# Kernel tuning notes

Hardware: AMD Instinct MI355X
Metric: run time of the kernel (lower is better)

## Reference

```python
import jax, jax.numpy as jnp
import numpy as np

Q, B, S, D, N = 4, 8, 1024, 768, 1024
H = 2 * D // 3  # 512, from encoder hidden = 2*dim//3
TAU = 1e-6      # eval-mode gumbel temperature
BN_EPS = 1e-5


def setup_inputs() -> dict:
    key = jax.random.key(0)
    ks = jax.random.split(key, 12)
    rn = lambda k, sh, sc=0.02: (jax.random.normal(k, sh, jnp.float32) * sc)
    u = jax.random.uniform(ks[0], (Q, B, S, N), jnp.float32, 1e-9, 1.0)
    return {
        "x": jax.random.normal(ks[1], (B, S, D), jnp.float32),
        "codebooks": rn(ks[2], (Q, N, D), 0.05),
        # posterior MLPs (per-quantizer, stacked over Q): Linear+BN(eval)+ReLU x2
        "pW1": rn(ks[3], (Q, D, H)), "pb1": jnp.zeros((Q, H)),
        "pg1": jnp.ones((Q, H)), "pbe1": jnp.zeros((Q, H)),
        "pm1": jnp.zeros((Q, H)), "pv1": jnp.ones((Q, H)),
        "pW2": rn(ks[4], (Q, H, N)), "pb2": jnp.zeros((Q, N)),
        "pg2": jnp.ones((Q, N)), "pbe2": jnp.zeros((Q, N)),
        "pm2": jnp.zeros((Q, N)), "pv2": jnp.ones((Q, N)),
        # shared decoder: D -> 2D -> D
        "dW1": rn(ks[5], (D, 2 * D)), "db1": jnp.zeros((2 * D,)),
        "dg1": jnp.ones((2 * D,)), "dbe1": jnp.zeros((2 * D,)),
        "dm1": jnp.zeros((2 * D,)), "dv1": jnp.ones((2 * D,)),
        "dW2": rn(ks[6], (2 * D, D)), "db2": jnp.zeros((D,)),
        "dg2": jnp.ones((D,)), "dbe2": jnp.zeros((D,)),
        "dm2": jnp.zeros((D,)), "dv2": jnp.ones((D,)),
        # precomputed gumbel noise (deterministic replacement for F.gumbel_softmax sampling)
        "gumbel": -jnp.log(-jnp.log(u)),
    }


def _bn(x, g, b, m, v):
    # eval-mode BatchNorm1d over the last (channel) axis
    return (x - m) * (g * jax.lax.rsqrt(v + BN_EPS)) + b


def _blk(x, W, b, g, be, m, v):
    return jax.nn.relu(_bn(x @ W + b, g, be, m, v))


def reference(x, codebooks, pW1, pb1, pg1, pbe1, pm1, pv1,
              pW2, pb2, pg2, pbe2, pm2, pv2,
              dW1, db1, dg1, dbe1, dm1, dv1,
              dW2, db2, dg2, dbe2, dm2, dv2, gumbel):
    residual = x
    quantized_out = jnp.zeros_like(x)
    indices, latent_losses, entropies, zs = [], [], [], []
    for i in range(Q):
        h = _blk(residual, pW1[i], pb1[i], pg1[i], pbe1[i], pm1[i], pv1[i])
        z = _blk(h, pW2[i], pb2[i], pg2[i], pbe2[i], pm2[i], pv2[i])  # [B,S,N]
        qy = jax.nn.softmax(z, axis=2)
        entropy = -jnp.sum(qy * jnp.log(qy + 1e-10), axis=-1)          # [B,S]
        latent = qy * jnp.log(qy * N + 1e-10)                           # [B,S,N]
        # gumbel-softmax, hard=True (straight-through)
        logits = (z + gumbel[i]) / TAU
        y_soft = jax.nn.softmax(logits, axis=2)
        idx = jnp.argmax(logits, axis=2)                                # [B,S]
        y_hard = jax.nn.one_hot(idx, N, dtype=z.dtype)
        one_hot = y_hard + y_soft - jax.lax.stop_gradient(y_soft)
        z_q = jnp.einsum('bsn,nd->bsd', one_hot, codebooks[i])
        residual = residual - jax.lax.stop_gradient(z_q)
        quantized_out = quantized_out + z_q
        indices.append(idx); latent_losses.append(latent)
        zs.append(z); entropies.append(entropy)
    h = _blk(quantized_out, dW1, db1, dg1, dbe1, dm1, dv1)
    xhat = _blk(h, dW2, db2, dg2, dbe2, dm2, dv2)
    return (xhat,
            jnp.stack(entropies, axis=0),
            jnp.stack(latent_losses, axis=0),
            jnp.stack(indices, axis=0),
            jnp.stack(zs, axis=0))
```

## Files before the change

kernel.cpp:

```cpp
#include <hip/hip_runtime.h>

namespace {

constexpr int QN = 4;
constexpr int MR = 8192;
constexpr int DD = 768;
constexpr int HH = 512;
constexpr int NN = 1024;
constexpr float DELTA = 0.008f;

typedef __attribute__((ext_vector_type(8))) __bf16 bf16x8;
typedef __attribute__((ext_vector_type(4))) __bf16 bf16x4;
typedef __attribute__((ext_vector_type(4))) float  f32x4;

#define GL2LDS(g, l) __builtin_amdgcn_global_load_lds( \
    (const __attribute__((address_space(1))) void*)(g), \
    (__attribute__((address_space(3))) void*)(l), 16, 0, 0)

__global__ __launch_bounds__(256)
void wcvt(const float* __restrict__ src, __bf16* __restrict__ dst, int K, int N)
{
    __shared__ float tile[32][33];
    const size_t bo = (size_t)blockIdx.z * K * N;
    const int n0 = blockIdx.x * 32, k0 = blockIdx.y * 32;
    const int tx = threadIdx.x, ty = threadIdx.y;
    #pragma unroll
    for (int i = 0; i < 4; ++i)
        tile[ty + 8 * i][tx] = src[bo + (size_t)(k0 + ty + 8 * i) * N + n0 + tx];
    __syncthreads();
    #pragma unroll
    for (int i = 0; i < 4; ++i)
        dst[bo + (size_t)(n0 + ty + 8 * i) * K + k0 + tx] = (__bf16)tile[tx][ty + 8 * i];
}

__global__ __launch_bounds__(256)
void acvt(const float* __restrict__ src, __bf16* __restrict__ dst,
          int* __restrict__ cnt)
{
    if (blockIdx.x == 0 && threadIdx.x < QN) cnt[threadIdx.x] = 0;
    const size_t i = ((size_t)blockIdx.x * 256 + threadIdx.x) * 8;
    float4 a = *(const float4*)(src + i);
    float4 b = *(const float4*)(src + i + 4);
    bf16x8 o;
    o[0] = (__bf16)a.x; o[1] = (__bf16)a.y; o[2] = (__bf16)a.z; o[3] = (__bf16)a.w;
    o[4] = (__bf16)b.x; o[5] = (__bf16)b.y; o[6] = (__bf16)b.z; o[7] = (__bf16)b.w;
    *(bf16x8*)(dst + i) = o;
}

template<int OUTBF>
__global__ __launch_bounds__(256)
void gemm_mfma(const __bf16* __restrict__ A, const __bf16* __restrict__ BT,
               const float* __restrict__ bias, const float* __restrict__ gam,
               const float* __restrict__ beta, const float* __restrict__ mean,
               const float* __restrict__ var,
               float* __restrict__ C32, __bf16* __restrict__ Cbf,
               int N_, int K_)
{
    __shared__ __bf16 smem[24576];

    const int t   = threadIdx.x;
    const int bn0 = blockIdx.x * 128;
    const int bm0 = blockIdx.y * 128;
    const int l    = t & 63, w = t >> 6;
    const int lm   = l & 15, quad = l >> 4;
    const int mrow = (w & 1) * 64, ncol = (w >> 1) * 64;

    const int sA0 = t, sA1 = t + 256;
    const int mA0 = sA0 >> 2, qA0 = ((sA0 & 3) - (mA0 >> 1)) & 3;
    const int mA1 = sA1 >> 2, qA1 = ((sA1 & 3) - (mA1 >> 1)) & 3;
    const size_t gA0 = (size_t)(bm0 + mA0) * K_ + qA0 * 8;
    const size_t gA1 = (size_t)(bm0 + mA1) * K_ + qA1 * 8;
    const size_t gB0 = (size_t)(bn0 + mA0) * K_ + qA0 * 8;
    const size_t gB1 = (size_t)(bn0 + mA1) * K_ + qA1 * 8;

    f32x4 acc[4][4] = {};

    int aslot[4], bslot[4];
    #pragma unroll
    for (int i = 0; i < 4; ++i) {
        int m = mrow + i * 16 + lm;
        aslot[i] = m * 4 + ((quad + (m >> 1)) & 3);
        int n = ncol + i * 16 + lm;
        bslot[i] = n * 4 + ((quad + (n >> 1)) & 3);
    }

    const int nk = K_ >> 5;

    {
        __bf16* As = smem;
        __bf16* Bs = smem + 4096;
        GL2LDS(A  + gA0, As + sA0 * 8);
        GL2LDS(A  + gA1, As + sA1 * 8);
        GL2LDS(BT + gB0, Bs + sA0 * 8);
        GL2LDS(BT + gB1, Bs + sA1 * 8);
        As = smem + 8192;
        Bs = As + 4096;
        GL2LDS(A  + gA0 + 32, As + sA0 * 8);
        GL2LDS(A  + gA1 + 32, As + sA1 * 8);
        GL2LDS(BT + gB0 + 32, Bs + sA0 * 8);
        GL2LDS(BT + gB1 + 32, Bs + sA1 * 8);
    }

    int bc = 0;
    for (int ks = 0; ks < nk; ++ks) {
        if (ks + 1 < nk) asm volatile("s_waitcnt vmcnt(4)" ::: "memory");
        else             asm volatile("s_waitcnt vmcnt(0)" ::: "memory");
        __builtin_amdgcn_s_barrier();
        asm volatile("" ::: "memory");

        if (ks + 2 < nk) {
            int sb = bc + 2; if (sb >= 3) sb -= 3;
            __bf16* Asn = smem + sb * 8192;
            __bf16* Bsn = Asn + 4096;
            const size_t ko = (size_t)(ks + 2) * 32;
            GL2LDS(A  + gA0 + ko, Asn + sA0 * 8);
            GL2LDS(A  + gA1 + ko, Asn + sA1 * 8);
            GL2LDS(BT + gB0 + ko, Bsn + sA0 * 8);
            GL2LDS(BT + gB1 + ko, Bsn + sA1 * 8);
        }

        const __bf16* As = smem + bc * 8192;
        const __bf16* Bs = As + 4096;
        bf16x8 af[4], bfv[4];
        #pragma unroll
        for (int i = 0; i < 4; ++i) {
            af[i]  = *(const bf16x8*)(As + aslot[i] * 8);
            bfv[i] = *(const bf16x8*)(Bs + bslot[i] * 8);
        }
        #pragma unroll
        for (int mt = 0; mt < 4; ++mt)
            #pragma unroll
            for (int nt = 0; nt < 4; ++nt)
                acc[mt][nt] = __builtin_amdgcn_mfma_f32_16x16x32_bf16(
                    af[mt], bfv[nt], acc[mt][nt], 0, 0, 0);

        asm volatile("s_waitcnt lgkmcnt(0)" ::: "memory");
        bc = (bc == 2) ? 0 : bc + 1;
    }

    float sc[4], sh[4]; int cn[4];
    #pragma unroll
    for (int nt = 0; nt < 4; ++nt) {
        int c = bn0 + ncol + nt * 16 + lm;
        cn[nt] = c;
        float s = gam[c] * rsqrtf(var[c] + 1e-5f);
        sc[nt] = s;
        sh[nt] = (bias[c] - mean[c]) * s + beta[c];
    }
    #pragma unroll
    for (int mt = 0; mt < 4; ++mt) {
        int r0 = bm0 + mrow + mt * 16 + quad * 4;
        #pragma unroll
        for (int nt = 0; nt < 4; ++nt) {
            #pragma unroll
            for (int reg = 0; reg < 4; ++reg) {
                float v = fmaxf(0.f, fmaf(acc[mt][nt][reg], sc[nt], sh[nt]));
                size_t off = (size_t)(r0 + reg) * N_ + cn[nt];
                if (OUTBF) Cbf[off] = (__bf16)v;
                else       C32[off] = v;
            }
        }
    }
}

__global__ __launch_bounds__(256)
void row_stats(const float* __restrict__ z, const float* __restrict__ gum,
               float* __restrict__ ent, float* __restrict__ lat,
               float* __restrict__ idxf,
               int* __restrict__ wl, int* __restrict__ cnt,
               const float* __restrict__ Ain, const float* __restrict__ cb,
               float* __restrict__ res, float* __restrict__ qout,
               __bf16* __restrict__ res_bf, __bf16* __restrict__ qo_bf,
               int first, int last)
{
    __shared__ float sred[8];
    __shared__ int   sredi[4];
    __shared__ float stop1;
    __shared__ int   stop1i;
    __shared__ int   sflag;

    const int r   = blockIdx.x;
    const int t   = threadIdx.x;
    const int wid = t >> 6;
    const bool l0 = (t & 63) == 0;

    const float4 z4 = ((const float4*)(z   + (size_t)r * NN))[t];
    const float4 g4 = ((const float4*)(gum + (size_t)r * NN))[t];

    float mx = fmaxf(fmaxf(z4.x, z4.y), fmaxf(z4.z, z4.w));
    #pragma unroll
    for (int o = 1; o < 64; o <<= 1) mx = fmaxf(mx, __shfl_xor(mx, o, 64));
    if (l0) sred[wid] = mx;
    __syncthreads();
    mx = fmaxf(fmaxf(sred[0], sred[1]), fmaxf(sred[2], sred[3]));

    float e0 = __expf(z4.x - mx), e1 = __expf(z4.y - mx);
    float e2 = __expf(z4.z - mx), e3 = __expf(z4.w - mx);
    float s = (e0 + e1) + (e2 + e3);
    #pragma unroll
    for (int o = 1; o < 64; o <<= 1) s += __shfl_xor(s, o, 64);
    if (l0) sred[4 + wid] = s;
    __syncthreads();
    s = (sred[4] + sred[5]) + (sred[6] + sred[7]);

    const float inv = 1.0f / s;
    const float q0 = e0 * inv, q1 = e1 * inv, q2 = e2 * inv, q3 = e3 * inv;

    float ep = q0 * __logf(q0 + 1e-10f) + q1 * __logf(q1 + 1e-10f)
             + q2 * __logf(q2 + 1e-10f) + q3 * __logf(q3 + 1e-10f);
    #pragma unroll
    for (int o = 1; o < 64; o <<= 1) ep += __shfl_xor(ep, o, 64);

    float4 l4;
    l4.x = q0 * __logf(q0 * 1024.f + 1e-10f);
    l4.y = q1 * __logf(q1 * 1024.f + 1e-10f);
    l4.z = q2 * __logf(q2 * 1024.f + 1e-10f);
    l4.w = q3 * __logf(q3 * 1024.f + 1e-10f);
    ((float4*)(lat + (size_t)r * NN))[t] = l4;

    const float y0 = z4.x + g4.x, y1 = z4.y + g4.y;
    const float y2 = z4.z + g4.z, y3 = z4.w + g4.w;
    float bv = y0; int bi = t * 4;
    if (y1 > bv) { bv = y1; bi = t * 4 + 1; }
    if (y2 > bv) { bv = y2; bi = t * 4 + 2; }
    if (y3 > bv) { bv = y3; bi = t * 4 + 3; }
    #pragma unroll
    for (int o = 1; o < 64; o <<= 1) {
        float ov = __shfl_xor(bv, o, 64);
        int   oi = __shfl_xor(bi, o, 64);
        if (ov > bv || (ov == bv && oi < bi)) { bv = ov; bi = oi; }
    }
    __syncthreads();
    if (l0) { sred[wid] = ep; sred[4 + wid] = bv; sredi[wid] = bi; }
    __syncthreads();
    if (t == 0) {
        ent[r] = -((sred[0] + sred[1]) + (sred[2] + sred[3]));
        float bbv = sred[4]; int bbi = sredi[0];
        #pragma unroll
        for (int ww = 1; ww < 4; ++ww)
            if (sred[4 + ww] > bbv || (sred[4 + ww] == bbv && sredi[ww] < bbi)) {
                bbv = sred[4 + ww]; bbi = sredi[ww];
            }
        stop1 = bbv; stop1i = bbi;
    }
    __syncthreads();
    const float t1v = stop1;
    const int   t1i = stop1i;

    float ex = -1e30f;
    if (t * 4 + 0 != t1i) ex = y0;
    if (t * 4 + 1 != t1i) ex = fmaxf(ex, y1);
    if (t * 4 + 2 != t1i) ex = fmaxf(ex, y2);
    if (t * 4 + 3 != t1i) ex = fmaxf(ex, y3);
    #pragma unroll
    for (int o = 1; o < 64; o <<= 1) ex = fmaxf(ex, __shfl_xor(ex, o, 64));
    __syncthreads();
    if (l0) sred[wid] = ex;
    __syncthreads();
    if (t == 0) {
        idxf[r] = (float)t1i;
        float t2 = fmaxf(fmaxf(sred[0], sred[1]), fmaxf(sred[2], sred[3]));
        int fl = (t1v - t2 < DELTA) ? 1 : 0;
        sflag = fl;
        if (fl) { int p = atomicAdd(cnt, 1); wl[p] = r; }
    }
    __syncthreads();

    if (!sflag && t < 192) {
        float4 c4 = *(const float4*)(cb + (size_t)t1i * DD + t * 4);
        float4 xv = *(const float4*)(Ain + (size_t)r * DD + t * 4);
        float4 rv, qv;
        rv.x = xv.x - c4.x; rv.y = xv.y - c4.y;
        rv.z = xv.z - c4.z; rv.w = xv.w - c4.w;
        if (first) { qv = c4; }
        else {
            qv = *(const float4*)(qout + (size_t)r * DD + t * 4);
            qv.x += c4.x; qv.y += c4.y; qv.z += c4.z; qv.w += c4.w;
        }
        if (!last) {
            *(float4*)(res  + (size_t)r * DD + t * 4) = rv;
            *(float4*)(qout + (size_t)r * DD + t * 4) = qv;
            bf16x4 rb;
            rb[0] = (__bf16)rv.x; rb[1] = (__bf16)rv.y;
            rb[2] = (__bf16)rv.z; rb[3] = (__bf16)rv.w;
            *(bf16x4*)(res_bf + (size_t)r * DD + t * 4) = rb;
        } else {
            bf16x4 qb;
            qb[0] = (__bf16)qv.x; qb[1] = (__bf16)qv.y;
            qb[2] = (__bf16)qv.z; qb[3] = (__bf16)qv.w;
            *(bf16x4*)(qo_bf + (size_t)r * DD + t * 4) = qb;
        }
    }
}

__global__ __launch_bounds__(256)
void recheck(const int* __restrict__ wl, const int* __restrict__ cnt,
             const float* __restrict__ gum, const float* __restrict__ Ain,
             const float* __restrict__ W1, const float* __restrict__ b1,
             const float* __restrict__ g1, const float* __restrict__ be1,
             const float* __restrict__ m1, const float* __restrict__ v1,
             const float* __restrict__ W2, const float* __restrict__ b2,
             const float* __restrict__ g2, const float* __restrict__ be2,
             const float* __restrict__ m2, const float* __restrict__ v2,
             float* __restrict__ idxf,
             const float* __restrict__ cb,
             float* __restrict__ res, float* __restrict__ qout,
             __bf16* __restrict__ res_bf, __bf16* __restrict__ qo_bf,
             int first, int last)
{
    __shared__ float rowbuf[DD];
    __shared__ float hs[HH];
    __shared__ float sred[4];
    __shared__ int   sredi[4];

    const int t   = threadIdx.x;
    const int wid = t >> 6;
    const bool l0 = (t & 63) == 0;
    const int n = cnt[0];

    for (int w = blockIdx.x; w < n; w += gridDim.x) {
        const int r = wl[w];
        __syncthreads();
        if (t < 192)
            *(float4*)&rowbuf[t * 4] = *(const float4*)(Ain + (size_t)r * DD + t * 4);
        __syncthreads();

        #pragma unroll
        for (int jj = 0; jj < 2; ++jj) {
            const int j = t + jj * 256;
            float a0 = 0.f, a1 = 0.f, a2 = 0.f, a3 = 0.f;
            #pragma unroll 4
            for (int k = 0; k < DD; k += 4) {
                a0 = fmaf(rowbuf[k + 0], W1[(size_t)(k + 0) * HH + j], a0);
                a1 = fmaf(rowbuf[k + 1], W1[(size_t)(k + 1) * HH + j], a1);
                a2 = fmaf(rowbuf[k + 2], W1[(size_t)(k + 2) * HH + j], a2);
                a3 = fmaf(rowbuf[k + 3], W1[(size_t)(k + 3) * HH + j], a3);
            }
            float a = (a0 + a1) + (a2 + a3) + b1[j];
            float scl = g1[j] * rsqrtf(v1[j] + 1e-5f);
            hs[j] = fmaxf(0.f, (a - m1[j]) * scl + be1[j]);
        }
        __syncthreads();

        float bv = -1e30f; int bi = 0;
        #pragma unroll
        for (int cc = 0; cc < 4; ++cc) {
            const int c = t + cc * 256;
            float a0 = 0.f, a1 = 0.f, a2 = 0.f, a3 = 0.f;
            #pragma unroll 4
            for (int j = 0; j < HH; j += 4) {
                a0 = fmaf(hs[j + 0], W2[(size_t)(j + 0) * NN + c], a0);
                a1 = fmaf(hs[j + 1], W2[(size_t)(j + 1) * NN + c], a1);
                a2 = fmaf(hs[j + 2], W2[(size_t)(j + 2) * NN + c], a2);
                a3 = fmaf(hs[j + 3], W2[(size_t)(j + 3) * NN + c], a3);
            }
            float a = (a0 + a1) + (a2 + a3) + b2[c];
            float scl = g2[c] * rsqrtf(v2[c] + 1e-5f);
            float zc  = fmaxf(0.f, (a - m2[c]) * scl + be2[c]);
            float y   = zc + gum[(size_t)r * NN + c];
            if (y > bv || (y == bv && c < bi)) { bv = y; bi = c; }
        }
        #pragma unroll
        for (int o = 1; o < 64; o <<= 1) {
            float ov = __shfl_xor(bv, o, 64);
            int   oi = __shfl_xor(bi, o, 64);
            if (ov > bv || (ov == bv && oi < bi)) { bv = ov; bi = oi; }
        }
        if (l0) { sred[wid] = bv; sredi[wid] = bi; }
        __syncthreads();
        if (t == 0) {
            float bbv = sred[0]; int bbi = sredi[0];
            #pragma unroll
            for (int ww = 1; ww < 4; ++ww)
                if (sred[ww] > bbv || (sred[ww] == bbv && sredi[ww] < bbi)) {
                    bbv = sred[ww]; bbi = sredi[ww];
                }
            idxf[r] = (float)bbi;
            sredi[0] = bbi;
        }
        __syncthreads();

        const int ci = sredi[0];
        if (t < 192) {
            float4 c4 = *(const float4*)(cb + (size_t)ci * DD + t * 4);
            float4 xv = *(const float4*)&rowbuf[t * 4];
            float4 rv, qv;
            rv.x = xv.x - c4.x; rv.y = xv.y - c4.y;
            rv.z = xv.z - c4.z; rv.w = xv.w - c4.w;
            if (first) { qv = c4; }
            else {
                qv = *(const float4*)(qout + (size_t)r * DD + t * 4);
                qv.x += c4.x; qv.y += c4.y; qv.z += c4.z; qv.w += c4.w;
            }
            if (!last) {
                *(float4*)(res  + (size_t)r * DD + t * 4) = rv;
                *(float4*)(qout + (size_t)r * DD + t * 4) = qv;
                bf16x4 rb;
                rb[0] = (__bf16)rv.x; rb[1] = (__bf16)rv.y;
                rb[2] = (__bf16)rv.z; rb[3] = (__bf16)rv.w;
                *(bf16x4*)(res_bf + (size_t)r * DD + t * 4) = rb;
            } else {
                bf16x4 qb;
                qb[0] = (__bf16)qv.x; qb[1] = (__bf16)qv.y;
                qb[2] = (__bf16)qv.z; qb[3] = (__bf16)qv.w;
                *(bf16x4*)(qo_bf + (size_t)r * DD + t * 4) = qb;
            }
        }
    }
}

}

extern "C" void kernel_launch(void* const* d_in, const int* in_sizes, int n_in,
                              void* d_out, int out_size, void* d_ws, size_t ws_size,
                              hipStream_t stream)
{
    const float* x    = (const float*)d_in[0];
    const float* cb   = (const float*)d_in[1];
    const float* pW1  = (const float*)d_in[2];
    const float* pb1  = (const float*)d_in[3];
    const float* pg1  = (const float*)d_in[4];
    const float* pbe1 = (const float*)d_in[5];
    const float* pm1  = (const float*)d_in[6];
    const float* pv1  = (const float*)d_in[7];
    const float* pW2  = (const float*)d_in[8];
    const float* pb2  = (const float*)d_in[9];
    const float* pg2  = (const float*)d_in[10];
    const float* pbe2 = (const float*)d_in[11];
    const float* pm2  = (const float*)d_in[12];
    const float* pv2  = (const float*)d_in[13];
    const float* dW1  = (const float*)d_in[14];
    const float* db1  = (const float*)d_in[15];
    const float* dg1  = (const float*)d_in[16];
    const float* dbe1 = (const float*)d_in[17];
    const float* dm1  = (const float*)d_in[18];
    const float* dv1  = (const float*)d_in[19];
    const float* dW2  = (const float*)d_in[20];
    const float* db2  = (const float*)d_in[21];
    const float* dg2  = (const float*)d_in[22];
    const float* dbe2 = (const float*)d_in[23];
    const float* dm2  = (const float*)d_in[24];
    const float* dv2  = (const float*)d_in[25];
    const float* gum  = (const float*)d_in[26];

    float* out  = (float*)d_out;
    float* xhat = out;
    float* ent  = xhat + (size_t)MR * DD;
    float* lat  = ent  + (size_t)QN * MR;
    float* idxf = lat  + (size_t)QN * MR * NN;
    float* zs   = idxf + (size_t)QN * MR;

    char* wp = (char*)d_ws;
    float*  res   = (float*)wp;                 wp += (size_t)MR * DD * 4;
    float*  qo    = (float*)wp;                 wp += (size_t)MR * DD * 4;
    __bf16* Abf   = (__bf16*)wp;                wp += (size_t)MR * DD * 2;
    __bf16* hbf   = (__bf16*)wp;                wp += (size_t)MR * HH * 2;
    __bf16* qobf  = (__bf16*)wp;                wp += (size_t)MR * DD * 2;
    __bf16* h1bf  = (__bf16*)wp;                wp += (size_t)MR * 2 * DD * 2;
    __bf16* w1t   = (__bf16*)wp;                wp += (size_t)QN * DD * HH * 2;
    __bf16* w2t   = (__bf16*)wp;                wp += (size_t)QN * HH * NN * 2;
    __bf16* dw1t  = (__bf16*)wp;                wp += (size_t)DD * 2 * DD * 2;
    __bf16* dw2t  = (__bf16*)wp;                wp += (size_t)2 * DD * DD * 2;
    int*    wl    = (int*)wp;                   wp += (size_t)QN * MR * 4;
    int*    cnt   = (int*)wp;                   wp += 64;

    dim3 b256(256), bwc(32, 8);

    hipLaunchKernelGGL(wcvt, dim3(HH / 32, DD / 32, QN), bwc, 0, stream, pW1, w1t, DD, HH);
    hipLaunchKernelGGL(wcvt, dim3(NN / 32, HH / 32, QN), bwc, 0, stream, pW2, w2t, HH, NN);
    hipLaunchKernelGGL(wcvt, dim3(2 * DD / 32, DD / 32, 1), bwc, 0, stream, dW1, dw1t, DD, 2 * DD);
    hipLaunchKernelGGL(wcvt, dim3(DD / 32, 2 * DD / 32, 1), bwc, 0, stream, dW2, dw2t, 2 * DD, DD);
    hipLaunchKernelGGL(acvt, dim3((size_t)MR * DD / (8 * 256)), b256, 0, stream, x, Abf, cnt);

    for (int i = 0; i < QN; ++i) {
        const int first = (i == 0), last = (i == QN - 1);
        hipLaunchKernelGGL((gemm_mfma<1>), dim3(HH / 128, MR / 128), b256, 0, stream,
            Abf, w1t + (size_t)i * DD * HH,
            pb1 + i * HH, pg1 + i * HH, pbe1 + i * HH, pm1 + i * HH, pv1 + i * HH,
            (float*)nullptr, hbf, HH, DD);
        float* z_i = zs + (size_t)i * MR * NN;
        hipLaunchKernelGGL((gemm_mfma<0>), dim3(NN / 128, MR / 128), b256, 0, stream,
            hbf, w2t + (size_t)i * HH * NN,
            pb2 + i * NN, pg2 + i * NN, pbe2 + i * NN, pm2 + i * NN, pv2 + i * NN,
            z_i, (__bf16*)nullptr, NN, HH);

        const float* Ain = (i == 0) ? x : res;
        hipLaunchKernelGGL(row_stats, dim3(MR), b256, 0, stream,
            z_i, gum + (size_t)i * MR * NN,
            ent + (size_t)i * MR, lat + (size_t)i * MR * NN, idxf + (size_t)i * MR,
            wl + (size_t)i * MR, cnt + i,
            Ain, cb + (size_t)i * NN * DD, res, qo, Abf, qobf, first, last);

        hipLaunchKernelGGL(recheck, dim3(256), b256, 0, stream,
            wl + (size_t)i * MR, cnt + i, gum + (size_t)i * MR * NN, Ain,
            pW1 + (size_t)i * DD * HH, pb1 + i * HH, pg1 + i * HH, pbe1 + i * HH,
            pm1 + i * HH, pv1 + i * HH,
            pW2 + (size_t)i * HH * NN, pb2 + i * NN, pg2 + i * NN, pbe2 + i * NN,
            pm2 + i * NN, pv2 + i * NN,
            idxf + (size_t)i * MR,
            cb + (size_t)i * NN * DD, res, qo, Abf, qobf, first, last);
    }
    hipLaunchKernelGGL((gemm_mfma<1>), dim3(2 * DD / 128, MR / 128), b256, 0, stream,
        qobf, dw1t, db1, dg1, dbe1, dm1, dv1, (float*)nullptr, h1bf, 2 * DD, DD);
    hipLaunchKernelGGL((gemm_mfma<0>), dim3(DD / 128, MR / 128), b256, 0, stream,
        h1bf, dw2t, db2, dg2, dbe2, dm2, dv2, xhat, (__bf16*)nullptr, DD, 2 * DD);
}
```

Measured before the change: 1.207 ms.

## Fuse near-tie fp32 recheck into row_stats and merge prep conversions into one launch

The four weight-transpose kernels and the activation conversion are merged into a single prep kernel that dispatches on block index. The separate recheck kernel, along with its atomic worklist and counter, is folded into row_stats. Each row whose top-two gumbel margin falls within DELTA now recomputes its MLP row in fp32 inline, and every row then applies the codebook update once. This removes five launches per call and the worklist traffic. The cost is that row_stats carries extra shared memory and a heavy divergent branch, and flagged rows now sit scattered across many blocks instead of a dense 256-block grid.

```diff
diff --git a/kernel.cpp b/kernel.cpp
--- a/kernel.cpp
+++ b/kernel.cpp
@@ -18,12 +18,47 @@
     (__attribute__((address_space(3))) void*)(l), 16, 0, 0)
 
 __global__ __launch_bounds__(256)
-void wcvt(const float* __restrict__ src, __bf16* __restrict__ dst, int K, int N)
+void prep(const float* __restrict__ pW1, const float* __restrict__ pW2,
+          const float* __restrict__ dW1, const float* __restrict__ dW2,
+          const float* __restrict__ x,
+          __bf16* __restrict__ w1t, __bf16* __restrict__ w2t,
+          __bf16* __restrict__ dw1t, __bf16* __restrict__ dw2t,
+          __bf16* __restrict__ Abf)
 {
+    const int id = blockIdx.x;
+    const int t  = threadIdx.x;
+
+    if (id >= 5888) {
+        const size_t i = ((size_t)(id - 5888) * 256 + t) * 8;
+        float4 a = *(const float4*)(x + i);
+        float4 b = *(const float4*)(x + i + 4);
+        bf16x8 o;
+        o[0] = (__bf16)a.x; o[1] = (__bf16)a.y; o[2] = (__bf16)a.z; o[3] = (__bf16)a.w;
+        o[4] = (__bf16)b.x; o[5] = (__bf16)b.y; o[6] = (__bf16)b.z; o[7] = (__bf16)b.w;
+        *(bf16x8*)(Abf + i) = o;
+        return;
+    }
+
     __shared__ float tile[32][33];
-    const size_t bo = (size_t)blockIdx.z * K * N;
-    const int n0 = blockIdx.x * 32, k0 = blockIdx.y * 32;
-    const int tx = threadIdx.x, ty = threadIdx.y;
+    const float* src; __bf16* dst; int K, N; size_t bo; int k0, n0;
+    if (id < 1536) {
+        int b = id / 384, rm = id % 384;
+        src = pW1; dst = w1t; K = 768; N = 512;
+        bo = (size_t)b * K * N; n0 = (rm & 15) * 32; k0 = (rm >> 4) * 32;
+    } else if (id < 3584) {
+        int q = id - 1536; int b = q / 512, rm = q % 512;
+        src = pW2; dst = w2t; K = 512; N = 1024;
+        bo = (size_t)b * K * N; n0 = (rm & 31) * 32; k0 = (rm >> 5) * 32;
+    } else if (id < 4736) {
+        int rm = id - 3584;
+        src = dW1; dst = dw1t; K = 768; N = 1536;
+        bo = 0; n0 = (rm % 48) * 32; k0 = (rm / 48) * 32;
+    } else {
+        int rm = id - 4736;
+        src = dW2; dst = dw2t; K = 1536; N = 768;
+        bo = 0; n0 = (rm % 24) * 32; k0 = (rm / 24) * 32;
+    }
+    const int tx = t & 31, ty = t >> 5;
     #pragma unroll
     for (int i = 0; i < 4; ++i)
         tile[ty + 8 * i][tx] = src[bo + (size_t)(k0 + ty + 8 * i) * N + n0 + tx];
@@ -31,20 +66,6 @@
     #pragma unroll
     for (int i = 0; i < 4; ++i)
         dst[bo + (size_t)(n0 + ty + 8 * i) * K + k0 + tx] = (__bf16)tile[tx][ty + 8 * i];
-}
-
-__global__ __launch_bounds__(256)
-void acvt(const float* __restrict__ src, __bf16* __restrict__ dst,
-          int* __restrict__ cnt)
-{
-    if (blockIdx.x == 0 && threadIdx.x < QN) cnt[threadIdx.x] = 0;
-    const size_t i = ((size_t)blockIdx.x * 256 + threadIdx.x) * 8;
-    float4 a = *(const float4*)(src + i);
-    float4 b = *(const float4*)(src + i + 4);
-    bf16x8 o;
-    o[0] = (__bf16)a.x; o[1] = (__bf16)a.y; o[2] = (__bf16)a.z; o[3] = (__bf16)a.w;
-    o[4] = (__bf16)b.x; o[5] = (__bf16)b.y; o[6] = (__bf16)b.z; o[7] = (__bf16)b.w;
-    *(bf16x8*)(dst + i) = o;
 }
 
 template<int OUTBF>
@@ -167,12 +188,19 @@
 void row_stats(const float* __restrict__ z, const float* __restrict__ gum,
                float* __restrict__ ent, float* __restrict__ lat,
                float* __restrict__ idxf,
-               int* __restrict__ wl, int* __restrict__ cnt,
                const float* __restrict__ Ain, const float* __restrict__ cb,
+               const float* __restrict__ W1, const float* __restrict__ b1,
+               const float* __restrict__ g1, const float* __restrict__ be1,
+               const float* __restrict__ m1, const float* __restrict__ v1,
+               const float* __restrict__ W2, const float* __restrict__ b2,
+               const float* __restrict__ g2, const float* __restrict__ be2,
+               const float* __restrict__ m2, const float* __restrict__ v2,
                float* __restrict__ res, float* __restrict__ qout,
                __bf16* __restrict__ res_bf, __bf16* __restrict__ qo_bf,
                int first, int last)
 {
+    __shared__ float rowbuf[DD];
+    __shared__ float hs[HH];
     __shared__ float sred[8];
     __shared__ int   sredi[4];
     __shared__ float stop1;
@@ -183,6 +211,9 @@
     const int t   = threadIdx.x;
     const int wid = t >> 6;
     const bool l0 = (t & 63) == 0;
+
+    if (t < 192)
+        *(float4*)&rowbuf[t * 4] = *(const float4*)(Ain + (size_t)r * DD + t * 4);
 
     const float4 z4 = ((const float4*)(z   + (size_t)r * NN))[t];
     const float4 g4 = ((const float4*)(gum + (size_t)r * NN))[t];
@@ -258,73 +289,14 @@
     if (l0) sred[wid] = ex;
     __syncthreads();
     if (t == 0) {
-        idxf[r] = (float)t1i;
         float t2 = fmaxf(fmaxf(sred[0], sred[1]), fmaxf(sred[2], sred[3]));
-        int fl = (t1v - t2 < DELTA) ? 1 : 0;
-        sflag = fl;
-        if (fl) { int p = atomicAdd(cnt, 1); wl[p] = r; }
-    }
-    __syncthreads();
-
-    if (!sflag && t < 192) {
-        float4 c4 = *(const float4*)(cb + (size_t)t1i * DD + t * 4);
-        float4 xv = *(const float4*)(Ain + (size_t)r * DD + t * 4);
-        float4 rv, qv;
-        rv.x = xv.x - c4.x; rv.y = xv.y - c4.y;
-        rv.z = xv.z - c4.z; rv.w = xv.w - c4.w;
-        if (first) { qv = c4; }
-        else {
-            qv = *(const float4*)(qout + (size_t)r * DD + t * 4);
-            qv.x += c4.x; qv.y += c4.y; qv.z += c4.z; qv.w += c4.w;
-        }
-        if (!last) {
-            *(float4*)(res  + (size_t)r * DD + t * 4) = rv;
-            *(float4*)(qout + (size_t)r * DD + t * 4) = qv;
-            bf16x4 rb;
-            rb[0] = (__bf16)rv.x; rb[1] = (__bf16)rv.y;
-            rb[2] = (__bf16)rv.z; rb[3] = (__bf16)rv.w;
-            *(bf16x4*)(res_bf + (size_t)r * DD + t * 4) = rb;
-        } else {
-            bf16x4 qb;
-            qb[0] = (__bf16)qv.x; qb[1] = (__bf16)qv.y;
-            qb[2] = (__bf16)qv.z; qb[3] = (__bf16)qv.w;
-            *(bf16x4*)(qo_bf + (size_t)r * DD + t * 4) = qb;
-        }
-    }
-}
-
-__global__ __launch_bounds__(256)
-void recheck(const int* __restrict__ wl, const int* __restrict__ cnt,
-             const float* __restrict__ gum, const float* __restrict__ Ain,
-             const float* __restrict__ W1, const float* __restrict__ b1,
-             const float* __restrict__ g1, const float* __restrict__ be1,
-             const float* __restrict__ m1, const float* __restrict__ v1,
-             const float* __restrict__ W2, const float* __restrict__ b2,
-             const float* __restrict__ g2, const float* __restrict__ be2,
-             const float* __restrict__ m2, const float* __restrict__ v2,
-             float* __restrict__ idxf,
-             const float* __restrict__ cb,
-             float* __restrict__ res, float* __restrict__ qout,
-             __bf16* __restrict__ res_bf, __bf16* __restrict__ qo_bf,
-             int first, int last)
-{
-    __shared__ float rowbuf[DD];
-    __shared__ float hs[HH];
-    __shared__ float sred[4];
-    __shared__ int   sredi[4];
-
-    const int t   = threadIdx.x;
-    const int wid = t >> 6;
-    const bool l0 = (t & 63) == 0;
-    const int n = cnt[0];
-
-    for (int w = blockIdx.x; w < n; w += gridDim.x) {
-        const int r = wl[w];
-        __syncthreads();
-        if (t < 192)
-            *(float4*)&rowbuf[t * 4] = *(const float4*)(Ain + (size_t)r * DD + t * 4);
-        __syncthreads();
-
+        sflag = (t1v - t2 < DELTA) ? 1 : 0;
+    }
+    __syncthreads();
+
+    int fidx = t1i;
+
+    if (sflag) {
         #pragma unroll
         for (int jj = 0; jj < 2; ++jj) {
             const int j = t + jj * 256;
@@ -342,7 +314,7 @@
         }
         __syncthreads();
 
-        float bv = -1e30f; int bi = 0;
+        float rbv = -1e30f; int rbi = 0;
         #pragma unroll
         for (int cc = 0; cc < 4; ++cc) {
             const int c = t + cc * 256;
@@ -358,15 +330,15 @@
             float scl = g2[c] * rsqrtf(v2[c] + 1e-5f);
             float zc  = fmaxf(0.f, (a - m2[c]) * scl + be2[c]);
             float y   = zc + gum[(size_t)r * NN + c];
-            if (y > bv || (y == bv && c < bi)) { bv = y; bi = c; }
+            if (y > rbv || (y == rbv && c < rbi)) { rbv = y; rbi = c; }
         }
         #pragma unroll
         for (int o = 1; o < 64; o <<= 1) {
-            float ov = __shfl_xor(bv, o, 64);
-            int   oi = __shfl_xor(bi, o, 64);
-            if (ov > bv || (ov == bv && oi < bi)) { bv = ov; bi = oi; }
-        }
-        if (l0) { sred[wid] = bv; sredi[wid] = bi; }
+            float ov = __shfl_xor(rbv, o, 64);
+            int   oi = __shfl_xor(rbi, o, 64);
+            if (ov > rbv || (ov == rbv && oi < rbi)) { rbv = ov; rbi = oi; }
+        }
+        if (l0) { sred[wid] = rbv; sredi[wid] = rbi; }
         __syncthreads();
         if (t == 0) {
             float bbv = sred[0]; int bbi = sredi[0];
@@ -375,36 +347,37 @@
                 if (sred[ww] > bbv || (sred[ww] == bbv && sredi[ww] < bbi)) {
                     bbv = sred[ww]; bbi = sredi[ww];
                 }
-            idxf[r] = (float)bbi;
-            sredi[0] = bbi;
+            stop1i = bbi;
         }
         __syncthreads();
-
-        const int ci = sredi[0];
-        if (t < 192) {
-            float4 c4 = *(const float4*)(cb + (size_t)ci * DD + t * 4);
-            float4 xv = *(const float4*)&rowbuf[t * 4];
-            float4 rv, qv;
-            rv.x = xv.x - c4.x; rv.y = xv.y - c4.y;
-            rv.z = xv.z - c4.z; rv.w = xv.w - c4.w;
-            if (first) { qv = c4; }
-            else {
-                qv = *(const float4*)(qout + (size_t)r * DD + t * 4);
-                qv.x += c4.x; qv.y += c4.y; qv.z += c4.z; qv.w += c4.w;
-            }
-            if (!last) {
-                *(float4*)(res  + (size_t)r * DD + t * 4) = rv;
-                *(float4*)(qout + (size_t)r * DD + t * 4) = qv;
-                bf16x4 rb;
-                rb[0] = (__bf16)rv.x; rb[1] = (__bf16)rv.y;
-                rb[2] = (__bf16)rv.z; rb[3] = (__bf16)rv.w;
-                *(bf16x4*)(res_bf + (size_t)r * DD + t * 4) = rb;
-            } else {
-                bf16x4 qb;
-                qb[0] = (__bf16)qv.x; qb[1] = (__bf16)qv.y;
-                qb[2] = (__bf16)qv.z; qb[3] = (__bf16)qv.w;
-                *(bf16x4*)(qo_bf + (size_t)r * DD + t * 4) = qb;
-            }
+        fidx = stop1i;
+    }
+
+    if (t == 0) idxf[r] = (float)fidx;
+
+    if (t < 192) {
+        float4 c4 = *(const float4*)(cb + (size_t)fidx * DD + t * 4);
+        float4 xv = *(const float4*)&rowbuf[t * 4];
+        float4 rv, qv;
+        rv.x = xv.x - c4.x; rv.y = xv.y - c4.y;
+        rv.z = xv.z - c4.z; rv.w = xv.w - c4.w;
+        if (first) { qv = c4; }
+        else {
+            qv = *(const float4*)(qout + (size_t)r * DD + t * 4);
+            qv.x += c4.x; qv.y += c4.y; qv.z += c4.z; qv.w += c4.w;
+        }
+        if (!last) {
+            *(float4*)(res  + (size_t)r * DD + t * 4) = rv;
+            *(float4*)(qout + (size_t)r * DD + t * 4) = qv;
+            bf16x4 rb;
+            rb[0] = (__bf16)rv.x; rb[1] = (__bf16)rv.y;
+            rb[2] = (__bf16)rv.z; rb[3] = (__bf16)rv.w;
+            *(bf16x4*)(res_bf + (size_t)r * DD + t * 4) = rb;
+        } else {
+            bf16x4 qb;
+            qb[0] = (__bf16)qv.x; qb[1] = (__bf16)qv.y;
+            qb[2] = (__bf16)qv.z; qb[3] = (__bf16)qv.w;
+            *(bf16x4*)(qo_bf + (size_t)r * DD + t * 4) = qb;
         }
     }
 }
@@ -461,16 +434,11 @@
     __bf16* w2t   = (__bf16*)wp;                wp += (size_t)QN * HH * NN * 2;
     __bf16* dw1t  = (__bf16*)wp;                wp += (size_t)DD * 2 * DD * 2;
     __bf16* dw2t  = (__bf16*)wp;                wp += (size_t)2 * DD * DD * 2;
-    int*    wl    = (int*)wp;                   wp += (size_t)QN * MR * 4;
-    int*    cnt   = (int*)wp;                   wp += 64;
-
-    dim3 b256(256), bwc(32, 8);
-
-    hipLaunchKernelGGL(wcvt, dim3(HH / 32, DD / 32, QN), bwc, 0, stream, pW1, w1t, DD, HH);
-    hipLaunchKernelGGL(wcvt, dim3(NN / 32, HH / 32, QN), bwc, 0, stream, pW2, w2t, HH, NN);
-    hipLaunchKernelGGL(wcvt, dim3(2 * DD / 32, DD / 32, 1), bwc, 0, stream, dW1, dw1t, DD, 2 * DD);
-    hipLaunchKernelGGL(wcvt, dim3(DD / 32, 2 * DD / 32, 1), bwc, 0, stream, dW2, dw2t, 2 * DD, DD);
-    hipLaunchKernelGGL(acvt, dim3((size_t)MR * DD / (8 * 256)), b256, 0, stream, x, Abf, cnt);
+
+    dim3 b256(256);
+
+    hipLaunchKernelGGL(prep, dim3(8960), b256, 0, stream,
+        pW1, pW2, dW1, dW2, x, w1t, w2t, dw1t, dw2t, Abf);
 
     for (int i = 0; i < QN; ++i) {
         const int first = (i == 0), last = (i == QN - 1);
@@ -488,17 +456,12 @@
         hipLaunchKernelGGL(row_stats, dim3(MR), b256, 0, stream,
             z_i, gum + (size_t)i * MR * NN,
             ent + (size_t)i * MR, lat + (size_t)i * MR * NN, idxf + (size_t)i * MR,
-            wl + (size_t)i * MR, cnt + i,
-            Ain, cb + (size_t)i * NN * DD, res, qo, Abf, qobf, first, last);
-
-        hipLaunchKernelGGL(recheck, dim3(256), b256, 0, stream,
-            wl + (size_t)i * MR, cnt + i, gum + (size_t)i * MR * NN, Ain,
+            Ain, cb + (size_t)i * NN * DD,
             pW1 + (size_t)i * DD * HH, pb1 + i * HH, pg1 + i * HH, pbe1 + i * HH,
             pm1 + i * HH, pv1 + i * HH,
             pW2 + (size_t)i * HH * NN, pb2 + i * NN, pg2 + i * NN, pbe2 + i * NN,
             pm2 + i * NN, pv2 + i * NN,
-            idxf + (size_t)i * MR,
-            cb + (size_t)i * NN * DD, res, qo, Abf, qobf, first, last);
+            res, qo, Abf, qobf, first, last);
     }
     hipLaunchKernelGGL((gemm_mfma<1>), dim3(2 * DD / 128, MR / 128), b256, 0, stream,
         qobf, dw1t, db1, dg1, dbe1, dm1, dv1, (float*)nullptr, h1bf, 2 * DD, DD);
```

Measured after the change: 1.230 ms. About the same (+1.9%).
